# Kernel tuning notes

Hardware: AMD Instinct MI355X
Metric: run time of the kernel (lower is better)

The kernel has to match this reference:

```python
import jax, jax.numpy as jnp
import numpy as np

B, S, E = 4, 2048, 1024
H = 16
D = E // H
WIN = 512


def setup_inputs() -> dict:
    key = jax.random.key(0)
    k1, k2, k3 = jax.random.split(key, 3)
    x = jax.random.normal(k1, (B, S, E), dtype=jnp.float32)
    w_in = jax.random.normal(k2, (3 * E, E), dtype=jnp.float32) * 0.02
    w_out = jax.random.normal(k3, (E, E), dtype=jnp.float32) * 0.02
    return {"x": x, "w_in": w_in, "w_out": w_out}


def _sliding_window_attention(q, k, v, win):
    b, h, s, d = q.shape
    nb = s // win
    scale = 1.0 / jnp.sqrt(jnp.float32(d))
    qb = q.reshape(b, h, nb, win, d)
    kb = k.reshape(b, h, nb, win, d)
    vb = v.reshape(b, h, nb, win, d)
    zpad = jnp.zeros_like(kb[:, :, :1])
    k2 = jnp.concatenate([jnp.concatenate([zpad, kb[:, :, :-1]], axis=2), kb], axis=3)  # [B,H,nb,2W,D]
    v2 = jnp.concatenate([jnp.concatenate([zpad, vb[:, :, :-1]], axis=2), vb], axis=3)
    scores = jnp.einsum('bhnqd,bhnkd->bhnqk', qb, k2) * scale  # [B,H,nb,W,2W]
    qi = jnp.arange(win)[:, None]          # query offset in block
    kj = jnp.arange(2 * win)[None, :]
    delta = qi - kj + win                  # q_idx - kv_idx
    valid = (delta >= 0) & (delta <= win)  # sliding-window causal mask
    blk = jnp.arange(nb)[:, None, None]
    valid = valid[None] & (blk * win + (kj[None] - win) >= 0)  # prev block invalid for block 0
    # ALiBi: bias = (q_idx - kv_idx) * exp2(-(h+1)*8/H)
    slopes = jnp.exp2(-(jnp.arange(H, dtype=jnp.float32) + 1.0) * 8.0 / H)  # [H]
    bias = slopes[:, None, None] * delta.astype(jnp.float32)  # [H,W,2W]
    scores = jnp.where(valid[None, :, :, :, :][:, None].squeeze(0)[None] if False else valid[None, None],
                       scores + bias[None, :, None], -jnp.inf)
    p = jax.nn.softmax(scores, axis=-1)
    out = jnp.einsum('bhnqk,bhnkd->bhnqd', p, v2)
    return out.reshape(b, h, s, d)


def reference(x, w_in, w_out):
    b, s, e = x.shape
    # packed in-projection (q is k is v path): split [3E,E] weight
    qkv = jnp.einsum('bse,fe->bsf', x, w_in)  # [B,S,3E]
    q, k, v = jnp.split(qkv, 3, axis=-1)
    def heads(t):
        return t.reshape(b, s, H, D).transpose(0, 2, 1, 3)  # [B,H,S,D]
    o = _sliding_window_attention(heads(q), heads(k), heads(v), WIN)  # [B,H,S,D]
    o = o.transpose(0, 2, 1, 3).reshape(b, s, e)
    return jnp.einsum('bse,fe->bsf', o, w_out)  # out_proj, batch-first output
```

## Files before the change

kernel.cpp:

```cpp
#include <hip/hip_runtime.h>
#include <hip/hip_bf16.h>


typedef __bf16 bf16x8 __attribute__((ext_vector_type(8)));
typedef __bf16 bf16x4 __attribute__((ext_vector_type(4)));
typedef short short4v __attribute__((ext_vector_type(4)));
typedef float f32x4 __attribute__((ext_vector_type(4)));

__device__ __forceinline__ f32x4 mfma16(bf16x8 a, bf16x8 b, f32x4 c) {
    return __builtin_amdgcn_mfma_f32_16x16x32_bf16(a, b, c, 0, 0, 0);
}

__device__ __forceinline__ f32x4 mfma16k16(bf16x4 a, bf16x4 b, f32x4 c) {
#if __has_builtin(__builtin_amdgcn_mfma_f32_16x16x16bf16_1k)
    return __builtin_amdgcn_mfma_f32_16x16x16bf16_1k(
        __builtin_bit_cast(short4v, a), __builtin_bit_cast(short4v, b), c, 0, 0, 0);
#elif __has_builtin(__builtin_amdgcn_mfma_f32_16x16x16_bf16)
    return __builtin_amdgcn_mfma_f32_16x16x16_bf16(a, b, c, 0, 0, 0);
#else
    asm("v_mfma_f32_16x16x16_bf16 %0, %1, %2, %0" : "+v"(c) : "v"(a), "v"(b));
    return c;
#endif
}

__device__ __forceinline__ void gload_lds16(const void* g, void* l) {
    __builtin_amdgcn_global_load_lds(
        (const __attribute__((address_space(1))) unsigned int*)(unsigned long long)g,
        (__attribute__((address_space(3))) unsigned int*)(unsigned int)(unsigned long long)l,
        16, 0, 0);
}

__device__ __forceinline__ unsigned pkbf(float a, float b) {
    unsigned short ua = __builtin_bit_cast(unsigned short, (__bf16)a);
    unsigned short ub = __builtin_bit_cast(unsigned short, (__bf16)b);
    return (unsigned)ua | ((unsigned)ub << 16);
}

__global__ void init_flag(int* flag) { *flag = 0; }

__global__ void detect_f32(const unsigned short* __restrict__ w, int n, int* flag) {
    int i = blockIdx.x * blockDim.x + threadIdx.x;
    int hit = 0;
    for (; i < n; i += gridDim.x * blockDim.x) {
        int e = (w[i] >> 7) & 0xFF;
        if (e >= 0x8D) hit = 1;
    }
    unsigned long long m = __ballot(hit);
    if (m != 0 && (threadIdx.x & 63) == 0) atomicOr(flag, 1);
}

__global__ void cvt_all(const void* __restrict__ x, const void* __restrict__ wi,
                        const void* __restrict__ wo, __bf16* __restrict__ xb,
                        __bf16* __restrict__ wib, __bf16* __restrict__ wob,
                        const int* __restrict__ flag) {
    if (*flag == 0) return;
    const int XN = 8192 * 1024, WI = 3072 * 1024, WO = 1024 * 1024;
    const int stride = gridDim.x * blockDim.x;
    int i0 = blockIdx.x * blockDim.x + threadIdx.x;
    for (int j = i0; j < XN; j += stride) xb[j] = (__bf16)((const float*)x)[j];
    for (int j = i0; j < WI; j += stride) wib[j] = (__bf16)((const float*)wi)[j];
    for (int j = i0; j < WO; j += stride) wob[j] = (__bf16)((const float*)wo)[j];
}

__global__ __launch_bounds__(256, 3) void gemm_bt(
        const void* __restrict__ Araw, const __bf16* __restrict__ Acvt,
        const void* __restrict__ Braw, const __bf16* __restrict__ Bcvt,
        __bf16* __restrict__ Cb, float* __restrict__ Cf,
        const int* __restrict__ flagp, int M, int N, int K) {
    __shared__ __align__(16) __bf16 As[128 * 64];
    __shared__ __align__(16) __bf16 Bs[128 * 64];

    const int t = threadIdx.x;
    const int lane = t & 63;
    const int w = t >> 6;
    const int wr = w >> 1, wc = w & 1;
    const int q4 = lane >> 4, l16 = lane & 15;
    const int m0 = blockIdx.y * 128, n0 = blockIdx.x * 128;
    const bool isf32 = (*flagp != 0);
    const __bf16* A = isf32 ? Acvt : (const __bf16*)Araw;
    const __bf16* Bt = isf32 ? Bcvt : (const __bf16*)Braw;

    f32x4 acc[4][4] = {};

    const int lr = lane >> 3;
    const int lc = (lane & 7) ^ lr;

    for (int k0 = 0; k0 < K; k0 += 64) {
#pragma unroll
        for (int p = 0; p < 4; ++p) {
            int r0 = w * 32 + p * 8;
            gload_lds16(&A[(size_t)(m0 + r0 + lr) * K + k0 + lc * 8], &As[r0 * 64]);
            gload_lds16(&Bt[(size_t)(n0 + r0 + lr) * K + k0 + lc * 8], &Bs[r0 * 64]);
        }
        __syncthreads();

#pragma unroll
        for (int kt = 0; kt < 2; ++kt) {
            bf16x8 af[4], bfr[4];
#pragma unroll
            for (int mt = 0; mt < 4; ++mt) {
                int row = wr * 64 + mt * 16 + l16;
                af[mt] = *(const bf16x8*)&As[row * 64 + (((kt * 4 + q4) ^ (row & 7)) << 3)];
            }
#pragma unroll
            for (int nt = 0; nt < 4; ++nt) {
                int row = wc * 64 + nt * 16 + l16;
                bfr[nt] = *(const bf16x8*)&Bs[row * 64 + (((kt * 4 + q4) ^ (row & 7)) << 3)];
            }
#pragma unroll
            for (int mt = 0; mt < 4; ++mt)
#pragma unroll
                for (int nt = 0; nt < 4; ++nt)
                    acc[mt][nt] = mfma16(af[mt], bfr[nt], acc[mt][nt]);
        }
        __syncthreads();
    }

#pragma unroll
    for (int mt = 0; mt < 4; ++mt)
#pragma unroll
        for (int nt = 0; nt < 4; ++nt) {
            int col = n0 + wc * 64 + nt * 16 + l16;
#pragma unroll
            for (int r = 0; r < 4; ++r) {
                int row = m0 + wr * 64 + mt * 16 + q4 * 4 + r;
                if (Cf && isf32)
                    Cf[(size_t)row * N + col] = acc[mt][nt][r];
                else
                    Cb[(size_t)row * N + col] = (__bf16)acc[mt][nt][r];
            }
        }
}

__global__ __launch_bounds__(256, 2) void attn(
        const __bf16* __restrict__ qkv, __bf16* __restrict__ o) {
    __shared__ __align__(16) char smem[2 * 17408];
    __bf16* Vts = (__bf16*)smem;
    __bf16* Ot  = (__bf16*)smem;

    const int qt = blockIdx.x, h = blockIdx.y, b = blockIdx.z;
    const int t = threadIdx.x;
    const int lane = t & 63, w = t >> 6;
    const int q4 = lane >> 4, l16 = lane & 15;
    const int q0 = qt * 128, qw0 = q0 + w * 32;

    const float L2E = 1.4426950408889634f;
    const float slope2 = exp2f(-(float)(h + 1) * 0.5f) * L2E;
    const float scale2 = L2E * 0.125f;

    const int srow = t >> 3, scb = t & 7;

    bf16x8 qf[2][2];
    const size_t qbase = ((size_t)b * 2048 + q0) * 3072 + (size_t)h * 64;
#pragma unroll
    for (int nt = 0; nt < 2; ++nt)
#pragma unroll
        for (int kt = 0; kt < 2; ++kt)
            qf[nt][kt] = *(const bf16x8*)&qkv[qbase +
                (size_t)(w * 32 + nt * 16 + l16) * 3072 + kt * 32 + q4 * 8];

    f32x4 O[4][2] = {};
    float mrow[2] = {-1e30f, -1e30f}, lrow[2] = {0.0f, 0.0f};

    const int nkt = (qt < 4 ? qt : 4) + 1;
    const int ktile0 = qt - (nkt - 1);
    const size_t bh = (size_t)b * 2048 * 3072 + (size_t)h * 64;
    const __bf16* Kg = qkv + bh + 1024 + (size_t)(q4 * 8);

    uint4 vpre[4];

    {
        const size_t vb = bh + (size_t)(ktile0 * 128) * 3072 + 2048;
#pragma unroll
        for (int p = 0; p < 4; ++p)
            vpre[p] = *(const uint4*)&qkv[vb + (size_t)(p * 32 + srow) * 3072 + scb * 8];
#pragma unroll
        for (int p = 0; p < 4; ++p) {
            const __bf16* ve = (const __bf16*)&vpre[p];
            int R = p * 4 + (srow >> 3);
#pragma unroll
            for (int j = 0; j < 8; ++j)
                Vts[(scb * 8 + j) * 136 + ((R ^ scb) << 3) + (srow & 7)] = ve[j];
        }
    }
    __syncthreads();

    for (int ki = 0; ki < nkt; ++ki) {
        const int k0 = (ktile0 + ki) * 128;
        const __bf16* Vb = Vts + (ki & 1) * 8704;
        if (ki + 1 < nkt) {
            const size_t vb = bh + (size_t)(k0 + 128) * 3072 + 2048;
#pragma unroll
            for (int p = 0; p < 4; ++p)
                vpre[p] = *(const uint4*)&qkv[vb + (size_t)(p * 32 + srow) * 3072 + scb * 8];
        }

#pragma unroll 1
        for (int hh = 0; hh < 2; ++hh) {
            const int ks0 = k0 + hh * 64;
            if (qw0 + 31 < ks0 || qw0 - 512 > ks0 + 63) continue;
            const bool interior = (qw0 - ks0 >= 63) && (qw0 - ks0 <= 481);

            f32x4 sc[2][4] = {};
#pragma unroll
            for (int mt = 0; mt < 4; ++mt) {
                const __bf16* kp = Kg + (size_t)(ks0 + mt * 16 + l16) * 3072;
                bf16x8 ak0 = *(const bf16x8*)kp;
                bf16x8 ak1 = *(const bf16x8*)(kp + 32);
                __builtin_amdgcn_s_setprio(1);
                sc[0][mt] = mfma16(ak0, qf[0][0], sc[0][mt]);
                sc[0][mt] = mfma16(ak1, qf[0][1], sc[0][mt]);
                sc[1][mt] = mfma16(ak0, qf[1][0], sc[1][mt]);
                sc[1][mt] = mfma16(ak1, qf[1][1], sc[1][mt]);
                __builtin_amdgcn_s_setprio(0);
            }

            uint2 pb[2][4];

#pragma unroll
            for (int nt = 0; nt < 2; ++nt) {
                const int qi = qw0 + nt * 16 + l16;
                const int db = qi - ks0 - q4 * 4;
                float tmx = -1e30f;
                if (interior) {
                    const float fb = slope2 * (float)db;
#pragma unroll
                    for (int mt = 0; mt < 4; ++mt) {
                        float bm = fb - (float)(16 * mt) * slope2;
#pragma unroll
                        for (int r = 0; r < 4; ++r) {
                            float v = fmaf(sc[nt][mt][r], scale2, bm - (float)r * slope2);
                            sc[nt][mt][r] = v;
                            tmx = fmaxf(tmx, v);
                        }
                    }
                } else {
#pragma unroll
                    for (int mt = 0; mt < 4; ++mt)
#pragma unroll
                        for (int r = 0; r < 4; ++r) {
                            int delta = db - mt * 16 - r;
                            float v = sc[nt][mt][r] * scale2 + slope2 * (float)delta;
                            v = ((unsigned)delta <= 512u) ? v : -1e30f;
                            sc[nt][mt][r] = v;
                            tmx = fmaxf(tmx, v);
                        }
                }
                tmx = fmaxf(tmx, __shfl_xor(tmx, 16));
                tmx = fmaxf(tmx, __shfl_xor(tmx, 32));

                if (__any(tmx > mrow[nt])) {
                    float mnew = fmaxf(mrow[nt], tmx);
                    float al = exp2f(mrow[nt] - mnew);
                    mrow[nt] = mnew;
                    lrow[nt] *= al;
#pragma unroll
                    for (int mtd = 0; mtd < 4; ++mtd)
                        O[mtd][nt] *= al;
                }

                float rs = 0.0f;
#pragma unroll
                for (int mt = 0; mt < 4; ++mt) {
                    float p0 = exp2f(sc[nt][mt][0] - mrow[nt]);
                    float p1 = exp2f(sc[nt][mt][1] - mrow[nt]);
                    float p2 = exp2f(sc[nt][mt][2] - mrow[nt]);
                    float p3 = exp2f(sc[nt][mt][3] - mrow[nt]);
                    rs += (p0 + p1) + (p2 + p3);
                    uint2 pk;
                    pk.x = pkbf(p0, p1);
                    pk.y = pkbf(p2, p3);
                    pb[nt][mt] = pk;
                }
                rs += __shfl_xor(rs, 16);
                rs += __shfl_xor(rs, 32);
                lrow[nt] += rs;
            }

            const int dsw = l16 >> 3;
#pragma unroll
            for (int mtB = 0; mtB < 4; ++mtB) {
                bf16x4 b0 = __builtin_bit_cast(bf16x4, pb[0][mtB]);
                bf16x4 b1 = __builtin_bit_cast(bf16x4, pb[1][mtB]);
                const int kc0 = hh * 8 + mtB * 2 + (q4 >> 1);
#pragma unroll
                for (int mtd = 0; mtd < 4; ++mtd) {
                    int kc = kc0 ^ ((mtd * 2 + dsw) & 7);
                    bf16x4 av = *(const bf16x4*)&Vb[(mtd * 16 + l16) * 136 +
                                                    (kc << 3) + (q4 & 1) * 4];
                    __builtin_amdgcn_s_setprio(1);
                    O[mtd][0] = mfma16k16(av, b0, O[mtd][0]);
                    O[mtd][1] = mfma16k16(av, b1, O[mtd][1]);
                    __builtin_amdgcn_s_setprio(0);
                }
            }
        }

        if (ki + 1 < nkt) {
            __bf16* Vn = Vts + ((ki + 1) & 1) * 8704;
#pragma unroll
            for (int p = 0; p < 4; ++p) {
                const __bf16* ve = (const __bf16*)&vpre[p];
                int R = p * 4 + (srow >> 3);
#pragma unroll
                for (int j = 0; j < 8; ++j)
                    Vn[(scb * 8 + j) * 136 + ((R ^ scb) << 3) + (srow & 7)] = ve[j];
            }
        }
        __syncthreads();
    }

#pragma unroll
    for (int nt = 0; nt < 2; ++nt) {
        float inv = (lrow[nt] > 0.0f) ? 1.0f / lrow[nt] : 0.0f;
        int qrow = w * 32 + nt * 16 + l16;
#pragma unroll
        for (int mtd = 0; mtd < 4; ++mtd) {
            int chunk = (mtd * 2 + (q4 >> 1)) ^ (l16 & 7);
            uint2 pk;
            pk.x = pkbf(O[mtd][nt][0] * inv, O[mtd][nt][1] * inv);
            pk.y = pkbf(O[mtd][nt][2] * inv, O[mtd][nt][3] * inv);
            *(uint2*)&Ot[qrow * 64 + (chunk << 3) + (q4 & 1) * 4] = pk;
        }
    }
    const size_t obase = ((size_t)b * 2048 + q0) * 1024 + (size_t)h * 64;
#pragma unroll
    for (int i = 0; i < 4; ++i) {
        int u = i * 64 + lane;
        int row = u >> 3, ch = u & 7;
        int q = w * 32 + row;
        *(uint4*)&o[obase + (size_t)q * 1024 + ch * 8] =
            *(const uint4*)&Ot[q * 64 + ((ch ^ (row & 7)) << 3)];
    }
}

extern "C" void kernel_launch(void* const* d_in, const int* in_sizes, int n_in,
                              void* d_out, int out_size, void* d_ws, size_t ws_size,
                              hipStream_t stream) {
    char* ws = (char*)d_ws;
    int* flag = (int*)ws;
    size_t off = 256;
    __bf16* xb  = (__bf16*)(ws + off); off += (size_t)8192 * 1024 * 2;
    __bf16* wib = (__bf16*)(ws + off); off += (size_t)3072 * 1024 * 2;
    __bf16* wob = (__bf16*)(ws + off); off += (size_t)1024 * 1024 * 2;
    __bf16* qkv = (__bf16*)(ws + off); off += (size_t)8192 * 3072 * 2;
    __bf16* o   = (__bf16*)(ws + off);

    init_flag<<<1, 1, 0, stream>>>(flag);
    int nscan = in_sizes[2] < 65536 ? in_sizes[2] : 65536;
    detect_f32<<<16, 256, 0, stream>>>((const unsigned short*)d_in[2], nscan, flag);
    cvt_all<<<1024, 256, 0, stream>>>(d_in[0], d_in[1], d_in[2], xb, wib, wob, flag);

    gemm_bt<<<dim3(24, 64), 256, 0, stream>>>(d_in[0], xb, d_in[1], wib,
                                              qkv, nullptr, flag, 8192, 3072, 1024);
    attn<<<dim3(16, 16, 4), 256, 0, stream>>>(qkv, o);
    gemm_bt<<<dim3(8, 64), 256, 0, stream>>>(o, o, d_in[2], wob,
                                             (__bf16*)d_out, (float*)d_out, flag,
                                             8192, 1024, 1024);
}
```

Measured before the change: 276.6 us.

## Stage K tiles in LDS via async global-to-LDS loads and remap attention grid

K tiles are now double-buffered in shared memory, loaded with direct global-to-LDS copies using an XOR swizzle, and read from LDS for the QK MFMAs, where before they were read per wave straight from global memory. The attention grid is flattened to 1D and remapped so neighbouring blocks share batch and head and walk adjacent query tiles, which should improve L2 reuse of K/V. Shared memory per block grows from about 34KB to about 67KB, which may limit occupancy under the two-blocks launch bound.

```diff
diff --git a/kernel.cpp b/kernel.cpp
--- a/kernel.cpp
+++ b/kernel.cpp
@@ -134,11 +134,17 @@
 
 __global__ __launch_bounds__(256, 2) void attn(
         const __bf16* __restrict__ qkv, __bf16* __restrict__ o) {
-    __shared__ __align__(16) char smem[2 * 17408];
-    __bf16* Vts = (__bf16*)smem;
+    __shared__ __align__(16) char smem[2 * 16384 + 2 * 17408];
+    __bf16* Ks  = (__bf16*)smem;
+    __bf16* Vts = (__bf16*)(smem + 32768);
     __bf16* Ot  = (__bf16*)smem;
 
-    const int qt = blockIdx.x, h = blockIdx.y, b = blockIdx.z;
+    const int L = blockIdx.x;
+    const int u = L & 255, v = L >> 8;
+    const int qt = v * 4 + (u & 3);
+    const int h  = (u >> 2) & 15;
+    const int b  = u >> 6;
+
     const int t = threadIdx.x;
     const int lane = t & 63, w = t >> 6;
     const int q4 = lane >> 4, l16 = lane & 15;
@@ -149,6 +155,8 @@
     const float scale2 = L2E * 0.125f;
 
     const int srow = t >> 3, scb = t & 7;
+    const int lr = lane >> 3;
+    const int lc = (lane & 7) ^ lr;
 
     bf16x8 qf[2][2];
     const size_t qbase = ((size_t)b * 2048 + q0) * 3072 + (size_t)h * 64;
@@ -165,15 +173,19 @@
     const int nkt = (qt < 4 ? qt : 4) + 1;
     const int ktile0 = qt - (nkt - 1);
     const size_t bh = (size_t)b * 2048 * 3072 + (size_t)h * 64;
-    const __bf16* Kg = qkv + bh + 1024 + (size_t)(q4 * 8);
 
     uint4 vpre[4];
 
     {
-        const size_t vb = bh + (size_t)(ktile0 * 128) * 3072 + 2048;
+        const size_t kb = bh + (size_t)(ktile0 * 128) * 3072 + 1024;
+#pragma unroll
+        for (int p = 0; p < 4; ++p) {
+            int r0 = w * 32 + p * 8;
+            gload_lds16(&qkv[kb + (size_t)(r0 + lr) * 3072 + lc * 8], &Ks[r0 * 64]);
+        }
 #pragma unroll
         for (int p = 0; p < 4; ++p)
-            vpre[p] = *(const uint4*)&qkv[vb + (size_t)(p * 32 + srow) * 3072 + scb * 8];
+            vpre[p] = *(const uint4*)&qkv[kb + 1024 + (size_t)(p * 32 + srow) * 3072 + scb * 8];
 #pragma unroll
         for (int p = 0; p < 4; ++p) {
             const __bf16* ve = (const __bf16*)&vpre[p];
@@ -187,12 +199,19 @@
 
     for (int ki = 0; ki < nkt; ++ki) {
         const int k0 = (ktile0 + ki) * 128;
+        const __bf16* Kb = Ks + (ki & 1) * 8192;
         const __bf16* Vb = Vts + (ki & 1) * 8704;
         if (ki + 1 < nkt) {
-            const size_t vb = bh + (size_t)(k0 + 128) * 3072 + 2048;
+            const size_t kb = bh + (size_t)(k0 + 128) * 3072 + 1024;
+            __bf16* Kn = Ks + ((ki + 1) & 1) * 8192;
+#pragma unroll
+            for (int p = 0; p < 4; ++p) {
+                int r0 = w * 32 + p * 8;
+                gload_lds16(&qkv[kb + (size_t)(r0 + lr) * 3072 + lc * 8], &Kn[r0 * 64]);
+            }
 #pragma unroll
             for (int p = 0; p < 4; ++p)
-                vpre[p] = *(const uint4*)&qkv[vb + (size_t)(p * 32 + srow) * 3072 + scb * 8];
+                vpre[p] = *(const uint4*)&qkv[kb + 1024 + (size_t)(p * 32 + srow) * 3072 + scb * 8];
         }
 
 #pragma unroll 1
@@ -204,9 +223,9 @@
             f32x4 sc[2][4] = {};
 #pragma unroll
             for (int mt = 0; mt < 4; ++mt) {
-                const __bf16* kp = Kg + (size_t)(ks0 + mt * 16 + l16) * 3072;
-                bf16x8 ak0 = *(const bf16x8*)kp;
-                bf16x8 ak1 = *(const bf16x8*)(kp + 32);
+                int krow = hh * 64 + mt * 16 + l16;
+                bf16x8 ak0 = *(const bf16x8*)&Kb[krow * 64 + ((q4 ^ (l16 & 7)) << 3)];
+                bf16x8 ak1 = *(const bf16x8*)&Kb[krow * 64 + (((4 + q4) ^ (l16 & 7)) << 3)];
                 __builtin_amdgcn_s_setprio(1);
                 sc[0][mt] = mfma16(ak0, qf[0][0], sc[0][mt]);
                 sc[0][mt] = mfma16(ak1, qf[0][1], sc[0][mt]);
@@ -326,8 +345,8 @@
     const size_t obase = ((size_t)b * 2048 + q0) * 1024 + (size_t)h * 64;
 #pragma unroll
     for (int i = 0; i < 4; ++i) {
-        int u = i * 64 + lane;
-        int row = u >> 3, ch = u & 7;
+        int u2 = i * 64 + lane;
+        int row = u2 >> 3, ch = u2 & 7;
         int q = w * 32 + row;
         *(uint4*)&o[obase + (size_t)q * 1024 + ch * 8] =
             *(const uint4*)&Ot[q * 64 + ((ch ^ (row & 7)) << 3)];
@@ -353,7 +372,7 @@
 
     gemm_bt<<<dim3(24, 64), 256, 0, stream>>>(d_in[0], xb, d_in[1], wib,
                                               qkv, nullptr, flag, 8192, 3072, 1024);
-    attn<<<dim3(16, 16, 4), 256, 0, stream>>>(qkv, o);
+    attn<<<dim3(1024), 256, 0, stream>>>(qkv, o);
     gemm_bt<<<dim3(8, 64), 256, 0, stream>>>(o, o, d_in[2], wob,
                                              (__bf16*)d_out, (float*)d_out, flag,
                                              8192, 1024, 1024);
```

Result: faster. 263.8 us (-4.6%).
